# Kernel optimization log

Hardware: AMD Instinct MI355X
Metric: run time of the kernel (lower is better)

The kernel has to match this reference:

```python
import jax, jax.numpy as jnp
import numpy as np

N = 100_000      # nodes
E = 1_600_000    # edges (before self-loops)
IN_C = 500
HID = 128
OUT_C = 64
L = 8
ALPHA = 0.1
THETA = 0.5


def setup_inputs() -> dict:
    key = jax.random.key(0)
    ks = jax.random.split(key, 6)
    x = jax.random.normal(ks[0], (N, IN_C), dtype=jnp.float32)
    edge_index = jax.random.randint(ks[1], (2, E), 0, N, dtype=jnp.int32)
    s0 = 1.0 / np.sqrt(IN_C)
    W_in = jax.random.uniform(ks[2], (IN_C, HID), jnp.float32, -s0, s0)
    b_in = jnp.zeros((HID,), jnp.float32)
    sh = 1.0 / np.sqrt(HID)
    W_conv = jax.random.uniform(ks[3], (L, HID, HID), jnp.float32, -sh, sh)
    W_out = jax.random.uniform(ks[4], (HID, OUT_C), jnp.float32, -sh, sh)
    b_out = jnp.zeros((OUT_C,), jnp.float32)
    return {"x": x, "edge_index": edge_index, "W_in": W_in, "b_in": b_in,
            "W_conv": W_conv, "W_out": W_out, "b_out": b_out}


def reference(x, edge_index, W_in, b_in, W_conv, W_out, b_out):
    # dropout is identity in eval mode
    loop = jnp.arange(N, dtype=edge_index.dtype)
    src = jnp.concatenate([edge_index[0], loop])  # add self-loops (gcn_norm)
    dst = jnp.concatenate([edge_index[1], loop])
    deg = jax.ops.segment_sum(jnp.ones_like(src, dtype=x.dtype), dst, num_segments=N)
    dinv = jnp.where(deg > 0, jax.lax.rsqrt(deg), 0.0)
    norm = dinv[src] * dinv[dst]  # symmetric normalization coeffs per edge

    h = jax.nn.relu(x @ W_in + b_in)
    h0 = h  # initial residual
    for l in range(L):
        beta = float(np.log(THETA / (l + 1) + 1.0))
        agg = jax.ops.segment_sum(h[src] * norm[:, None], dst, num_segments=N)  # Ahat @ h
        z = (1.0 - ALPHA) * agg + ALPHA * h0
        h = jax.nn.relu((1.0 - beta) * z + beta * (z @ W_conv[l]))
    return h @ W_out + b_out
```

## Files before the change

kernel.cpp:

```cpp
#include <hip/hip_runtime.h>
#include <hip/hip_fp16.h>
#include <cmath>

#define NN 100000
#define EE 1600000
#define INC 500
#define HIDC 128
#define OUTC 64
#define NLAYER 8
#define NB16 6250
#define NPX 12500
#define CNT_BLKS 50000
#define NBLK 391

typedef float f32x4 __attribute__((ext_vector_type(4)));
typedef _Float16 f16x8 __attribute__((ext_vector_type(8)));
typedef short s16x8 __attribute__((ext_vector_type(8)));

__device__ __forceinline__ int fraddr(int row, int k, int Kp) {
  return (row >> 4) * (Kp * 16) + (k >> 3) * 128 + (row & 15) * 8 + (k & 7);
}


__global__ void __launch_bounds__(256) k_count_x(
    const int* __restrict__ dst, int* __restrict__ deg) {
  int chunk = blockIdx.x >> 3;
  int xcd = blockIdx.x & 7;
  int e = chunk * 256 + threadIdx.x;
  int d = dst[e];
  if (d / NPX == xcd) atomicAdd(&deg[d], 1);
}

__global__ void k_scan_block_sums(const int* __restrict__ deg, int* __restrict__ bsum, int n) {
  __shared__ int sm[256];
  int i = blockIdx.x * 256 + threadIdx.x;
  int v = (i < n) ? deg[i] + 1 : 0;
  sm[threadIdx.x] = v;
  __syncthreads();
  for (int s = 128; s > 0; s >>= 1) {
    if (threadIdx.x < s) sm[threadIdx.x] += sm[threadIdx.x + s];
    __syncthreads();
  }
  if (threadIdx.x == 0) bsum[blockIdx.x] = sm[0];
}

__global__ void k_scan_partials(int* __restrict__ bsum, int nb) {
  __shared__ int sm[512];
  int t = threadIdx.x;
  sm[t] = (t < nb) ? bsum[t] : 0;
  __syncthreads();
  for (int s = 1; s < 512; s <<= 1) {
    int v = (t >= s) ? sm[t - s] : 0;
    __syncthreads();
    sm[t] += v;
    __syncthreads();
  }
  if (t < nb) bsum[t] = (t == 0) ? 0 : sm[t - 1];
}

__global__ void k_scan_final(const int* __restrict__ deg, const int* __restrict__ bsum,
                             int* __restrict__ row_ptr, int n) {
  __shared__ int sm[256];
  int i = blockIdx.x * 256 + threadIdx.x;
  int v = (i < n) ? deg[i] + 1 : 0;
  sm[threadIdx.x] = v;
  __syncthreads();
  for (int s = 1; s < 256; s <<= 1) {
    int u = (threadIdx.x >= s) ? sm[threadIdx.x - s] : 0;
    __syncthreads();
    sm[threadIdx.x] += u;
    __syncthreads();
  }
  if (i < n) row_ptr[i] = bsum[blockIdx.x] + sm[threadIdx.x] - v;
}

__global__ void k_init_rows(const int* __restrict__ deg, const int* __restrict__ row_ptr,
                            int* __restrict__ cursor, int* __restrict__ col,
                            float* __restrict__ dinv, int n) {
  int i = blockIdx.x * blockDim.x + threadIdx.x;
  if (i < n) {
    int rp = row_ptr[i];
    col[rp] = i;
    cursor[i] = rp + 1;
    dinv[i] = rsqrtf((float)(deg[i] + 1));
  }
}

__global__ void __launch_bounds__(256) k_fill_x(
    const int* __restrict__ src, const int* __restrict__ dst,
    int* __restrict__ cursor, int* __restrict__ col) {
  int chunk = blockIdx.x >> 3;
  int xcd = blockIdx.x & 7;
  int e = chunk * 256 + threadIdx.x;
  int d = dst[e];
  if (d / NPX == xcd) {
    int pos = atomicAdd(&cursor[d], 1);
    col[pos] = src[e];
  }
}


__global__ void k_prep_wfin16(const float* __restrict__ W, __half* __restrict__ f) {
  int i = blockIdx.x * 256 + threadIdx.x;
  if (i >= HIDC * 512) return;
  int n = i / 512, k = i % 512;
  float v = (k < INC) ? W[(size_t)k * HIDC + n] : 0.f;
  f[fraddr(n, k, 512)] = __float2half(v);
}


__global__ void k_prep_wf16(const float* __restrict__ W, __half* __restrict__ f,
                            int K, int N, float idc, float ws) {
  int i = blockIdx.x * 256 + threadIdx.x;
  if (i >= N * K) return;
  int n = i / K, k = i % K;
  float v = ws * W[(size_t)k * N + n] + ((k == n) ? idc : 0.f);
  f[fraddr(n, k, K)] = __float2half(v);
}


__global__ void __launch_bounds__(256) k_gemm_in(
    const float* __restrict__ A, const __half* __restrict__ Bf,
    const float* __restrict__ bias,
    __half* __restrict__ C16u, __half* __restrict__ C16s,
    const float* __restrict__ dinv) {
  int wv = threadIdx.x >> 6, lane = threadIdx.x & 63;
  int lr = lane & 15, kg = lane >> 4;
  int w16 = blockIdx.x * 4 + wv;
  if (w16 >= NB16) return;
  int row = w16 * 16 + lr;

  f32x4 acc[8];
#pragma unroll
  for (int n = 0; n < 8; ++n) acc[n] = {0.f, 0.f, 0.f, 0.f};

  const float* Ar = A + (size_t)row * INC;
  const __half* Bb = Bf + lr * 8;

  float4 pa0[4], pa1[4];

  auto loadA = [&](int kt, float4& d0, float4& d1) {
    int k0 = kt * 32 + kg * 8;
    if (kt < 15 || kg < 2) {
      d0 = *reinterpret_cast<const float4*>(Ar + k0);
      d1 = *reinterpret_cast<const float4*>(Ar + k0 + 4);
    } else {
      float t[8];
#pragma unroll
      for (int e = 0; e < 8; ++e) t[e] = (k0 + e < INC) ? Ar[k0 + e] : 0.f;
      d0 = make_float4(t[0], t[1], t[2], t[3]);
      d1 = make_float4(t[4], t[5], t[6], t[7]);
    }
  };

#pragma unroll
  for (int d = 0; d < 4; ++d) loadA(d, pa0[d], pa1[d]);

#pragma unroll
  for (int kt = 0; kt < 16; ++kt) {
    float4 a0 = pa0[kt & 3], a1 = pa1[kt & 3];
    if (kt + 4 < 16) loadA(kt + 4, pa0[kt & 3], pa1[kt & 3]);
    f16x8 af;
    af[0] = (_Float16)a0.x; af[1] = (_Float16)a0.y;
    af[2] = (_Float16)a0.z; af[3] = (_Float16)a0.w;
    af[4] = (_Float16)a1.x; af[5] = (_Float16)a1.y;
    af[6] = (_Float16)a1.z; af[7] = (_Float16)a1.w;
    int kslab = (kt * 4 + kg) * 128;
#pragma unroll
    for (int n = 0; n < 8; ++n) {
      f16x8 b = *reinterpret_cast<const f16x8*>(&Bb[n * 8192 + kslab]);
      acc[n] = __builtin_amdgcn_mfma_f32_16x16x32_f16(af, b, acc[n], 0, 0, 0);
    }
  }

#pragma unroll
  for (int q = 0; q < 4; ++q) {
    int gr = w16 * 16 + kg * 4 + q;
    float dv = dinv[gr];
#pragma unroll
    for (int n = 0; n < 8; ++n) {
      int gc = n * 16 + lr;
      float v = fmaxf(acc[n][q] + bias[gc], 0.f);
      C16u[(size_t)gr * HIDC + gc] = __float2half(v);
      C16s[(size_t)gr * HIDC + gc] = __float2half(v * dv);
    }
  }
}


template <int EPI>
__global__ void __launch_bounds__(1024) k_layer(
    const __half* __restrict__ hs, const __half* __restrict__ h0u,
    const __half* __restrict__ Bf,
    const int* __restrict__ row_ptr, const int* __restrict__ deg,
    const int* __restrict__ col, const float* __restrict__ dinv,
    __half* __restrict__ Cs,
    const __half* __restrict__ Bf2, const float* __restrict__ bias2,
    float* __restrict__ outp) {
  __shared__ __half zb[16 * 128];
  int wv = threadIdx.x >> 6, lane = threadIdx.x & 63;
  int g = lane >> 4;
  int fl = lane & 15;
  int row0 = blockIdx.x * 16;
  int node = row0 + wv;

  int start = row_ptr[node];
  int cnt = deg[node] + 1;

  float acc[8];
#pragma unroll
  for (int j = 0; j < 8; ++j) acc[j] = 0.f;

  for (int base = 0; base < cnt; base += 64) {
    int rem = cnt - base;
    if (rem > 64) rem = 64;
    int myc = col[start + base + (lane < rem ? lane : 0)];
    int nch = (rem + 3) >> 2;

    auto get = [&](int ch, s16x8& v, float& m) {
      int e = ch * 4 + g;
      int c = __shfl(myc, e & 63, 64);
      m = (e < rem) ? 1.f : 0.f;
      v = *reinterpret_cast<const s16x8*>(&hs[(size_t)c * HIDC + fl * 8]);
    };

    s16x8 curv; float curm;
    get(0, curv, curm);
    for (int ch = 0; ch < nch; ++ch) {
      s16x8 nv = {}; float nm = 0.f;
      if (ch + 1 < nch) get(ch + 1, nv, nm);
      const __half2* hp = reinterpret_cast<const __half2*>(&curv);
#pragma unroll
      for (int j = 0; j < 4; ++j) {
        float2 f = __half22float2(hp[j]);
        acc[2 * j]     = fmaf(curm, f.x, acc[2 * j]);
        acc[2 * j + 1] = fmaf(curm, f.y, acc[2 * j + 1]);
      }
      curv = nv; curm = nm;
    }
  }

#pragma unroll
  for (int j = 0; j < 8; ++j) {
    acc[j] += __shfl_xor(acc[j], 16, 64);
    acc[j] += __shfl_xor(acc[j], 32, 64);
  }

  if (g == 0) {
    float dr = dinv[node] * 0.9f;
    s16x8 r0 = *reinterpret_cast<const s16x8*>(&h0u[(size_t)node * HIDC + fl * 8]);
    const __half2* r0p = reinterpret_cast<const __half2*>(&r0);
    f16x8 w;
#pragma unroll
    for (int j = 0; j < 4; ++j) {
      float2 f0 = __half22float2(r0p[j]);
      w[2 * j]     = (_Float16)fmaf(dr, acc[2 * j],     0.1f * f0.x);
      w[2 * j + 1] = (_Float16)fmaf(dr, acc[2 * j + 1], 0.1f * f0.y);
    }
    *reinterpret_cast<f16x8*>(&zb[wv * 128 + ((fl * 8) ^ ((wv & 7) << 3))]) = w;
  }
  __syncthreads();

  int lr = lane & 15, kg = lane >> 4;
  f32x4 c = {0.f, 0.f, 0.f, 0.f};
  if (wv < 8) {
    const __half* Bb = Bf + wv * 2048 + kg * 128 + lr * 8;
#pragma unroll
    for (int kt = 0; kt < 4; ++kt) {
      f16x8 a = *reinterpret_cast<const f16x8*>(
          &zb[lr * 128 + ((kt * 32 + kg * 8) ^ ((lr & 7) << 3))]);
      f16x8 b = *reinterpret_cast<const f16x8*>(Bb + kt * 512);
      c = __builtin_amdgcn_mfma_f32_16x16x32_f16(a, b, c, 0, 0, 0);
    }
  }

  if (EPI == 0) {
    if (wv < 8) {
      int gc = wv * 16 + lr;
#pragma unroll
      for (int q = 0; q < 4; ++q) {
        int gr = row0 + kg * 4 + q;
        float v = fmaxf(c[q], 0.f);
        Cs[(size_t)gr * HIDC + gc] = __float2half(v * dinv[gr]);
      }
    }
  } else {
    __syncthreads();
    if (wv < 8) {
      int gc = wv * 16 + lr;
#pragma unroll
      for (int q = 0; q < 4; ++q) {
        int r = kg * 4 + q;
        zb[(gc >> 3) * 128 + r * 8 + (gc & 7)] = __float2half(fmaxf(c[q], 0.f));
      }
    }
    __syncthreads();
    if (wv < 4) {
      f32x4 o = {0.f, 0.f, 0.f, 0.f};
      const __half* Bb2 = Bf2 + wv * 2048 + kg * 128 + lr * 8;
#pragma unroll
      for (int kt = 0; kt < 4; ++kt) {
        f16x8 a = *reinterpret_cast<const f16x8*>(&zb[(kt * 4 + kg) * 128 + lr * 8]);
        f16x8 b = *reinterpret_cast<const f16x8*>(Bb2 + kt * 512);
        o = __builtin_amdgcn_mfma_f32_16x16x32_f16(a, b, o, 0, 0, 0);
      }
      int gc = wv * 16 + lr;
      float bv = bias2[gc];
#pragma unroll
      for (int q = 0; q < 4; ++q) {
        int gr = row0 + kg * 4 + q;
        outp[(size_t)gr * OUTC + gc] = o[q] + bv;
      }
    }
  }
}


extern "C" void kernel_launch(void* const* d_in, const int* in_sizes, int n_in,
                              void* d_out, int out_size, void* d_ws, size_t ws_size,
                              hipStream_t stream) {
  const float* x     = (const float*)d_in[0];
  const int*   ei    = (const int*)d_in[1];
  const float* W_in  = (const float*)d_in[2];
  const float* b_in  = (const float*)d_in[3];
  const float* W_cv  = (const float*)d_in[4];
  const float* W_out = (const float*)d_in[5];
  const float* b_out = (const float*)d_in[6];
  float* out = (float*)d_out;

  char* ws = (char*)d_ws;
  size_t off = 0;
  auto alloc = [&](size_t bytes) {
    char* p = ws + off;
    off = (off + bytes + 255) & ~(size_t)255;
    return p;
  };
  int*    deg     = (int*)alloc((size_t)NN * 4);
  int*    row_ptr = (int*)alloc((size_t)NN * 4);
  int*    cursor  = (int*)alloc((size_t)NN * 4);
  int*    bsum    = (int*)alloc(512 * 4);
  float*  dinv    = (float*)alloc((size_t)NN * 4);
  int*    col     = (int*)alloc((size_t)(EE + NN) * 4);
  __half* h016u   = (__half*)alloc((size_t)NN * HIDC * 2);
  __half* h016s   = (__half*)alloc((size_t)NN * HIDC * 2);
  __half* hsA     = (__half*)alloc((size_t)NN * HIDC * 2);
  __half* hsB     = (__half*)alloc((size_t)NN * HIDC * 2);
  __half* wcv16   = (__half*)alloc((size_t)NLAYER * HIDC * HIDC * 2);
  __half* wout16  = (__half*)alloc((size_t)OUTC * HIDC * 2);
  __half* win16   = (__half*)alloc((size_t)HIDC * 512 * 2);

  const int* srcp = ei;
  const int* dstp = ei + EE;

  hipMemsetAsync(deg, 0, (size_t)NN * 4, stream);

  k_prep_wfin16<<<(HIDC * 512 + 255) / 256, 256, 0, stream>>>(W_in, win16);
  for (int l = 0; l < NLAYER; ++l) {
    float beta = logf(0.5f / (float)(l + 1) + 1.0f);
    k_prep_wf16<<<(HIDC * HIDC + 255) / 256, 256, 0, stream>>>(
        W_cv + (size_t)l * HIDC * HIDC, wcv16 + (size_t)l * HIDC * HIDC,
        HIDC, HIDC, 1.0f - beta, beta);
  }
  k_prep_wf16<<<(OUTC * HIDC + 255) / 256, 256, 0, stream>>>(W_out, wout16, HIDC, OUTC,
                                                             0.f, 1.f);

  k_count_x<<<CNT_BLKS, 256, 0, stream>>>(dstp, deg);

  k_scan_block_sums<<<NBLK, 256, 0, stream>>>(deg, bsum, NN);
  k_scan_partials<<<1, 512, 0, stream>>>(bsum, NBLK);
  k_scan_final<<<NBLK, 256, 0, stream>>>(deg, bsum, row_ptr, NN);
  k_init_rows<<<(NN + 255) / 256, 256, 0, stream>>>(deg, row_ptr, cursor, col, dinv, NN);

  k_fill_x<<<CNT_BLKS, 256, 0, stream>>>(srcp, dstp, cursor, col);

  k_gemm_in<<<(NB16 + 3) / 4, 256, 0, stream>>>(x, win16, b_in, h016u, h016s, dinv);

  const __half* hcur = h016s;
  for (int l = 0; l < NLAYER; ++l) {
    const __half* wl = wcv16 + (size_t)l * HIDC * HIDC;
    if (l < NLAYER - 1) {
      __half* tgt = (l & 1) ? hsB : hsA;
      k_layer<0><<<NB16, 1024, 0, stream>>>(hcur, h016u, wl, row_ptr, deg, col, dinv,
                                            tgt, nullptr, nullptr, nullptr);
      hcur = tgt;
    } else {
      k_layer<1><<<NB16, 1024, 0, stream>>>(hcur, h016u, wl, row_ptr, deg, col, dinv,
                                            nullptr, wout16, b_out, out);
    }
  }
}
```

Baseline: 905.2 us.

## Sort nodes by degree within 256-node windows to balance per-block aggregation work

```diff
diff --git a/kernel.cpp b/kernel.cpp
--- a/kernel.cpp
+++ b/kernel.cpp
@@ -12,6 +12,7 @@
 #define NPX 12500
 #define CNT_BLKS 50000
 #define NBLK 391
+#define PERMSZ (NBLK * 256)
 
 typedef float f32x4 __attribute__((ext_vector_type(4)));
 typedef _Float16 f16x8 __attribute__((ext_vector_type(8)));
@@ -84,6 +85,29 @@
     cursor[i] = rp + 1;
     dinv[i] = rsqrtf((float)(deg[i] + 1));
   }
+}
+
+
+__global__ void __launch_bounds__(256) k_sort_win(
+    const int* __restrict__ deg, int* __restrict__ perm) {
+  __shared__ unsigned key[256];
+  int t = threadIdx.x;
+  int base = blockIdx.x * 256;
+  int node = base + t;
+  key[t] = (node < NN) ? (((unsigned)deg[node] << 18) | (unsigned)t) : 0xFFFFFFFFu;
+  __syncthreads();
+  for (int sz = 2; sz <= 256; sz <<= 1) {
+    for (int st = sz >> 1; st > 0; st >>= 1) {
+      int p = t ^ st;
+      if (p > t) {
+        unsigned a = key[t], b = key[p];
+        bool asc = ((t & sz) == 0);
+        if (asc ? (a > b) : (a < b)) { key[t] = b; key[p] = a; }
+      }
+      __syncthreads();
+    }
+  }
+  perm[base + t] = base + (int)(key[t] & 0x3FFFFu);
 }
 
 __global__ void __launch_bounds__(256) k_fill_x(
@@ -158,6 +182,11 @@
 
 #pragma unroll
   for (int kt = 0; kt < 16; ++kt) {
+    int kslab = (kt * 4 + kg) * 128;
+    f16x8 bfr[8];
+#pragma unroll
+    for (int n = 0; n < 8; ++n)
+      bfr[n] = *reinterpret_cast<const f16x8*>(&Bb[n * 8192 + kslab]);
     float4 a0 = pa0[kt & 3], a1 = pa1[kt & 3];
     if (kt + 4 < 16) loadA(kt + 4, pa0[kt & 3], pa1[kt & 3]);
     f16x8 af;
@@ -165,12 +194,9 @@
     af[2] = (_Float16)a0.z; af[3] = (_Float16)a0.w;
     af[4] = (_Float16)a1.x; af[5] = (_Float16)a1.y;
     af[6] = (_Float16)a1.z; af[7] = (_Float16)a1.w;
-    int kslab = (kt * 4 + kg) * 128;
-#pragma unroll
-    for (int n = 0; n < 8; ++n) {
-      f16x8 b = *reinterpret_cast<const f16x8*>(&Bb[n * 8192 + kslab]);
-      acc[n] = __builtin_amdgcn_mfma_f32_16x16x32_f16(af, b, acc[n], 0, 0, 0);
-    }
+#pragma unroll
+    for (int n = 0; n < 8; ++n)
+      acc[n] = __builtin_amdgcn_mfma_f32_16x16x32_f16(af, bfr[n], acc[n], 0, 0, 0);
   }
 
 #pragma unroll
@@ -194,6 +220,7 @@
     const __half* __restrict__ Bf,
     const int* __restrict__ row_ptr, const int* __restrict__ deg,
     const int* __restrict__ col, const float* __restrict__ dinv,
+    const int* __restrict__ perm,
     __half* __restrict__ Cs,
     const __half* __restrict__ Bf2, const float* __restrict__ bias2,
     float* __restrict__ outp) {
@@ -202,7 +229,7 @@
   int g = lane >> 4;
   int fl = lane & 15;
   int row0 = blockIdx.x * 16;
-  int node = row0 + wv;
+  int node = perm[row0 + wv];
 
   int start = row_ptr[node];
   int cnt = deg[node] + 1;
@@ -279,9 +306,9 @@
       int gc = wv * 16 + lr;
 #pragma unroll
       for (int q = 0; q < 4; ++q) {
-        int gr = row0 + kg * 4 + q;
+        int pr = perm[row0 + kg * 4 + q];
         float v = fmaxf(c[q], 0.f);
-        Cs[(size_t)gr * HIDC + gc] = __float2half(v * dinv[gr]);
+        Cs[(size_t)pr * HIDC + gc] = __float2half(v * dinv[pr]);
       }
     }
   } else {
@@ -308,8 +335,8 @@
       float bv = bias2[gc];
 #pragma unroll
       for (int q = 0; q < 4; ++q) {
-        int gr = row0 + kg * 4 + q;
-        outp[(size_t)gr * OUTC + gc] = o[q] + bv;
+        int pr = perm[row0 + kg * 4 + q];
+        outp[(size_t)pr * OUTC + gc] = o[q] + bv;
       }
     }
   }
@@ -339,6 +366,7 @@
   int*    row_ptr = (int*)alloc((size_t)NN * 4);
   int*    cursor  = (int*)alloc((size_t)NN * 4);
   int*    bsum    = (int*)alloc(512 * 4);
+  int*    perm    = (int*)alloc((size_t)PERMSZ * 4);
   float*  dinv    = (float*)alloc((size_t)NN * 4);
   int*    col     = (int*)alloc((size_t)(EE + NN) * 4);
   __half* h016u   = (__half*)alloc((size_t)NN * HIDC * 2);
@@ -371,6 +399,8 @@
   k_scan_final<<<NBLK, 256, 0, stream>>>(deg, bsum, row_ptr, NN);
   k_init_rows<<<(NN + 255) / 256, 256, 0, stream>>>(deg, row_ptr, cursor, col, dinv, NN);
 
+  k_sort_win<<<NBLK, 256, 0, stream>>>(deg, perm);
+
   k_fill_x<<<CNT_BLKS, 256, 0, stream>>>(srcp, dstp, cursor, col);
 
   k_gemm_in<<<(NB16 + 3) / 4, 256, 0, stream>>>(x, win16, b_in, h016u, h016s, dinv);
@@ -381,11 +411,11 @@
     if (l < NLAYER - 1) {
       __half* tgt = (l & 1) ? hsB : hsA;
       k_layer<0><<<NB16, 1024, 0, stream>>>(hcur, h016u, wl, row_ptr, deg, col, dinv,
-                                            tgt, nullptr, nullptr, nullptr);
+                                            perm, tgt, nullptr, nullptr, nullptr);
       hcur = tgt;
     } else {
       k_layer<1><<<NB16, 1024, 0, stream>>>(hcur, h016u, wl, row_ptr, deg, col, dinv,
-                                            nullptr, wout16, b_out, out);
-    }
-  }
-}
+                                            perm, nullptr, wout16, b_out, out);
+    }
+  }
+}
```

Measured after the change: 1.031 ms. 13.9% more time.
